# Performance work log

Measured on AMD Instinct MI355X. Metric: run time of the kernel, lower is better.

The kernel has to match this reference:

```python
import jax, jax.numpy as jnp
import numpy as np

N_NODES = 50000
N_EDGES = 1_600_000
DIMS = [3, 4096, 1024, 256, 64, 16]  # conv1..conv5 in/out widths


def setup_inputs() -> dict:
    key = jax.random.key(0)
    ks = jax.random.split(key, 2 + 2 * 6)
    x = jax.random.normal(ks[0], (N_NODES, DIMS[0]), jnp.float32)
    edge_index = jax.random.randint(ks[1], (2, N_EDGES), 0, N_NODES, jnp.int64)
    inp = {"x": x, "edge_index": edge_index}
    # GCNConv weights (lin has no bias fused; bias added after aggregation)
    for i in range(5):
        fi, fo = DIMS[i], DIMS[i + 1]
        inp[f"W{i+1}"] = jax.random.normal(ks[2 + 2 * i], (fi, fo), jnp.float32) / np.float32(np.sqrt(fi))
        inp[f"b{i+1}"] = jnp.zeros((fo,), jnp.float32)
    # final Linear(num_classes, 3)
    inp["Wl"] = jax.random.normal(ks[12], (DIMS[5], 3), jnp.float32) / np.float32(np.sqrt(DIMS[5]))
    inp["bl"] = jnp.zeros((3,), jnp.float32)
    return inp


def _gcn_layer(x, W, b, src, dst, dinv):
    """GCNConv: h = XW; out = D^-1/2 (A+I) D^-1/2 h + b (self-loops included)."""
    h = x @ W  # [N, out]
    norm = dinv[src] * dinv[dst]  # [E]
    agg = jax.ops.segment_sum(h[src] * norm[:, None], dst, num_segments=N_NODES)
    # self-loop term: norm_ii = dinv[i]^2
    return agg + h * (dinv * dinv)[:, None] + b


def reference(x, edge_index, W1, b1, W2, b2, W3, b3, W4, b4, W5, b5, Wl, bl):
    src, dst = edge_index[0], edge_index[1]
    # degree with self-loops (edge weights = 1), computed on target nodes
    deg = jax.ops.segment_sum(jnp.ones((N_EDGES,), x.dtype), dst, num_segments=N_NODES) + 1.0
    dinv = jax.lax.rsqrt(deg)
    h = _gcn_layer(x, W1, b1, src, dst, dinv)
    h = jax.nn.relu(h)  # dropout = identity in eval
    h = _gcn_layer(h, W2, b2, src, dst, dinv)
    h = jax.nn.relu(h)
    h = _gcn_layer(h, W3, b3, src, dst, dinv)
    h = jax.nn.relu(h)
    h = _gcn_layer(h, W4, b4, src, dst, dinv)
    h = jax.nn.relu(h)
    h = _gcn_layer(h, W5, b5, src, dst, dinv)
    # scatter_mean with broadcast index [0] -> global mean pool to [1, C]
    pooled = jnp.mean(h, axis=0, keepdims=True)
    return pooled @ Wl + bl  # [1, 3]
```

## Files before the change

### kernel.cpp

```cpp
#include <hip/hip_runtime.h>
#include <stdint.h>

#define NN 50000
#define NE 1600000

typedef _Float16 f16;
typedef __attribute__((ext_vector_type(8))) _Float16 h8;
typedef __attribute__((ext_vector_type(4))) _Float16 h4v;
typedef __attribute__((ext_vector_type(4))) float f32x4;
typedef __attribute__((ext_vector_type(2))) float f32x2;

union PackU { unsigned int u; f16 h[2]; };
union Pack4 { uint2 v; f16 h[4]; };
union Pack8 { uint4 v; f16 h[8]; };

__device__ __forceinline__ void storev(float* p, float v) { *p = v; }
__device__ __forceinline__ void storev(f16* p, float v) { *p = (f16)v; }

__device__ __forceinline__ unsigned char f2fp8(float v) {
    int pk = __builtin_amdgcn_cvt_pk_fp8_f32(v, v, 0, false);
    return (unsigned char)(pk & 0xff);
}

__global__ __launch_bounds__(256) void zero_int_kernel(int* __restrict__ p, int n) {
    int i = blockIdx.x * 256 + threadIdx.x;
    if (i < n) p[i] = 0;
}

__global__ __launch_bounds__(256) void count_kernel(const int* __restrict__ dst,
                                                    int* __restrict__ deg, int nE) {
    int e = blockIdx.x * 256 + threadIdx.x;
    if (e < nE) atomicAdd(&deg[dst[e]], 1);
}

__global__ __launch_bounds__(256) void dinv_kernel(const int* __restrict__ deg,
                                                   float* __restrict__ dinv, int n) {
    int i = blockIdx.x * 256 + threadIdx.x;
    if (i < n) dinv[i] = rsqrtf((float)deg[i] + 1.0f);
}

__global__ __launch_bounds__(256) void scan1_kernel(const int* __restrict__ cnt,
                                                    int* __restrict__ rs,
                                                    int* __restrict__ bsum, int n) {
    __shared__ int sm[256];
    int b = blockIdx.x, t = threadIdx.x, i = b * 256 + t;
    int v = (i < n) ? cnt[i] : 0;
    sm[t] = v;
    __syncthreads();
    for (int off = 1; off < 256; off <<= 1) {
        int x = 0;
        if (t >= off) x = sm[t - off];
        __syncthreads();
        if (t >= off) sm[t] += x;
        __syncthreads();
    }
    if (i < n) rs[i] = sm[t] - v;
    if (t == 255) bsum[b] = sm[255];
}

__global__ __launch_bounds__(256) void scan2_kernel(int* __restrict__ bsum,
                                                    int* __restrict__ rs, int nb, int n) {
    __shared__ int sm[256];
    int t = threadIdx.x;
    int v = (t < nb) ? bsum[t] : 0;
    sm[t] = v;
    __syncthreads();
    for (int off = 1; off < 256; off <<= 1) {
        int x = 0;
        if (t >= off) x = sm[t - off];
        __syncthreads();
        if (t >= off) sm[t] += x;
        __syncthreads();
    }
    if (t < nb) bsum[t] = sm[t] - v;
    if (t == 255) rs[n] = sm[255];
}

__global__ __launch_bounds__(256) void scan3_kernel(int* __restrict__ rs,
                                                    const int* __restrict__ bsum, int n) {
    int i = blockIdx.x * 256 + threadIdx.x;
    if (i < n) rs[i] += bsum[blockIdx.x];
}

__global__ __launch_bounds__(256) void fill_kernel(const int* __restrict__ src,
                                                   const int* __restrict__ dst,
                                                   const int* __restrict__ rs,
                                                   int* __restrict__ cur,
                                                   int* __restrict__ csr, int nE) {
    int e = blockIdx.x * 256 + threadIdx.x;
    if (e < nE) {
        int d = dst[e];
        int p = rs[d] + atomicAdd(&cur[d], 1);
        csr[p] = src[e];
    }
}

__global__ __launch_bounds__(256) void pack_w1_kernel(const float* __restrict__ W1,
                                                      const float* __restrict__ b1,
                                                      float* __restrict__ w1p) {
    int k = blockIdx.x * 256 + threadIdx.x;
    if (k < 4096) {
        w1p[k * 4 + 0] = W1[k];
        w1p[k * 4 + 1] = W1[4096 + k];
        w1p[k * 4 + 2] = W1[8192 + k];
        w1p[k * 4 + 3] = b1[k];
    }
}

__global__ __launch_bounds__(256) void tconv_kernel(const float* __restrict__ W,
                                                    f16* __restrict__ Wt,
                                                    int K, int N) {
    __shared__ float tile[32][33];
    int kb = blockIdx.y * 32, nb = blockIdx.x * 32;
    int tx = threadIdx.x & 31, ty = threadIdx.x >> 5;
    for (int r = ty; r < 32; r += 8)
        tile[r][tx] = W[(size_t)(kb + r) * N + nb + tx];
    __syncthreads();
    for (int r = ty; r < 32; r += 8)
        Wt[(size_t)(nb + r) * K + kb + tx] = (f16)tile[tx][r];
}

template <int F, int TPN, bool RELU, bool BIAS, typename InT, typename OutT>
__global__ __launch_bounds__(256) void agg_kernel(const InT* __restrict__ t,
                                                  const float* __restrict__ dinv,
                                                  const int* __restrict__ rs,
                                                  const int* __restrict__ csr,
                                                  const float* __restrict__ bias,
                                                  OutT* __restrict__ out, int out_ld,
                                                  int nNodes) {
    constexpr int NPB = 256 / TPN;
    constexpr int C   = F / TPN;
    static_assert(TPN * C == F, "F must be TPN*C");
    int node = blockIdx.x * NPB + (int)threadIdx.x / TPN;
    if (node >= nNodes) return;
    int lane = (int)threadIdx.x % TPN;

    float acc[C];
#pragma unroll
    for (int c = 0; c < C; ++c) acc[c] = 0.f;

    int e0 = rs[node], e1 = rs[node + 1];
    for (int e = e0; e < e1; ++e) {
        int s = csr[e];
        float w = dinv[s];
        const InT* tr = t + (size_t)s * F;
#pragma unroll
        for (int c = 0; c < C; ++c) acc[c] += w * (float)tr[lane + c * TPN];
    }
    float di = dinv[node];
    const InT* ti = t + (size_t)node * F;
    OutT* oi = out + (size_t)node * out_ld;
#pragma unroll
    for (int c = 0; c < C; ++c) {
        int col = lane + c * TPN;
        float v = di * acc[c] + di * di * (float)ti[col];
        if (BIAS) v += bias[col];
        if (RELU) v = fmaxf(v, 0.f);
        storev(oi + col, v);
    }
}

template <bool RELU>
__global__ __launch_bounds__(256) void agg_fp8_1024(const unsigned char* __restrict__ t,
                                                    const float* __restrict__ dinv,
                                                    const int* __restrict__ rs,
                                                    const int* __restrict__ csr,
                                                    const float* __restrict__ bias,
                                                    f16* __restrict__ out, int nNodes) {
    int node = blockIdx.x * 4 + ((int)threadIdx.x >> 6);
    if (node >= nNodes) return;
    int lane = (int)threadIdx.x & 63;

    float acc[16];
#pragma unroll
    for (int j = 0; j < 16; ++j) acc[j] = 0.f;

    int e0 = rs[node], e1 = rs[node + 1];
    int e = e0;
    for (; e + 1 < e1; e += 2) {
        int s0 = csr[e], s1 = csr[e + 1];
        float w0 = dinv[s0], w1 = dinv[s1];
        uint4 u0 = ((const uint4*)(t + (size_t)s0 * 1024))[lane];
        uint4 u1 = ((const uint4*)(t + (size_t)s1 * 1024))[lane];
        const unsigned int uw0[4] = {u0.x, u0.y, u0.z, u0.w};
        const unsigned int uw1[4] = {u1.x, u1.y, u1.z, u1.w};
#pragma unroll
        for (int q = 0; q < 4; ++q) {
            f32x2 l0 = __builtin_amdgcn_cvt_pk_f32_fp8((int)uw0[q], false);
            f32x2 h0 = __builtin_amdgcn_cvt_pk_f32_fp8((int)uw0[q], true);
            f32x2 l1 = __builtin_amdgcn_cvt_pk_f32_fp8((int)uw1[q], false);
            f32x2 h1 = __builtin_amdgcn_cvt_pk_f32_fp8((int)uw1[q], true);
            acc[q * 4 + 0] += w0 * l0.x + w1 * l1.x;
            acc[q * 4 + 1] += w0 * l0.y + w1 * l1.y;
            acc[q * 4 + 2] += w0 * h0.x + w1 * h1.x;
            acc[q * 4 + 3] += w0 * h0.y + w1 * h1.y;
        }
    }
    if (e < e1) {
        int s0 = csr[e];
        float w0 = dinv[s0];
        uint4 u0 = ((const uint4*)(t + (size_t)s0 * 1024))[lane];
        const unsigned int uw0[4] = {u0.x, u0.y, u0.z, u0.w};
#pragma unroll
        for (int q = 0; q < 4; ++q) {
            f32x2 l0 = __builtin_amdgcn_cvt_pk_f32_fp8((int)uw0[q], false);
            f32x2 h0 = __builtin_amdgcn_cvt_pk_f32_fp8((int)uw0[q], true);
            acc[q * 4 + 0] += w0 * l0.x;
            acc[q * 4 + 1] += w0 * l0.y;
            acc[q * 4 + 2] += w0 * h0.x;
            acc[q * 4 + 3] += w0 * h0.y;
        }
    }
    float di = dinv[node], di2 = di * di;
    uint4 us = ((const uint4*)(t + (size_t)node * 1024))[lane];
    const unsigned int uws[4] = {us.x, us.y, us.z, us.w};
    Pack8 o0, o1;
#pragma unroll
    for (int q = 0; q < 4; ++q) {
        f32x2 sl = __builtin_amdgcn_cvt_pk_f32_fp8((int)uws[q], false);
        f32x2 sh = __builtin_amdgcn_cvt_pk_f32_fp8((int)uws[q], true);
        float4 b = *(const float4*)(bias + 16 * lane + q * 4);
        float v0 = di * acc[q * 4 + 0] + di2 * sl.x + b.x;
        float v1 = di * acc[q * 4 + 1] + di2 * sl.y + b.y;
        float v2 = di * acc[q * 4 + 2] + di2 * sh.x + b.z;
        float v3 = di * acc[q * 4 + 3] + di2 * sh.y + b.w;
        if (RELU) {
            v0 = fmaxf(v0, 0.f); v1 = fmaxf(v1, 0.f);
            v2 = fmaxf(v2, 0.f); v3 = fmaxf(v3, 0.f);
        }
        Pack8& dst8 = (q < 2) ? o0 : o1;
        int base = (q & 1) * 4;
        dst8.h[base + 0] = (f16)v0;
        dst8.h[base + 1] = (f16)v1;
        dst8.h[base + 2] = (f16)v2;
        dst8.h[base + 3] = (f16)v3;
    }
    uint4* orow = (uint4*)(out + (size_t)node * 1024 + 16 * lane);
    orow[0] = o0.v;
    orow[1] = o1.v;
}

template <bool RELU>
__global__ __launch_bounds__(256) void agg_fp8_256(const unsigned char* __restrict__ t,
                                                   int in_ld,
                                                   const float* __restrict__ dinv,
                                                   const int* __restrict__ rs,
                                                   const int* __restrict__ csr,
                                                   const float* __restrict__ bias,
                                                   f16* __restrict__ out,
                                                   int out_ld, int nNodes) {
    int node = blockIdx.x * 4 + ((int)threadIdx.x >> 6);
    if (node >= nNodes) return;
    int lane = (int)threadIdx.x & 63;

    float acc0 = 0.f, acc1 = 0.f, acc2 = 0.f, acc3 = 0.f;
    int e0 = rs[node], e1 = rs[node + 1];
    int e = e0;
    for (; e + 1 < e1; e += 2) {
        int s0 = csr[e], s1 = csr[e + 1];
        float w0 = dinv[s0], w1 = dinv[s1];
        unsigned int u0 = ((const unsigned int*)(t + (size_t)s0 * in_ld))[lane];
        unsigned int u1 = ((const unsigned int*)(t + (size_t)s1 * in_ld))[lane];
        f32x2 l0 = __builtin_amdgcn_cvt_pk_f32_fp8((int)u0, false);
        f32x2 h0 = __builtin_amdgcn_cvt_pk_f32_fp8((int)u0, true);
        f32x2 l1 = __builtin_amdgcn_cvt_pk_f32_fp8((int)u1, false);
        f32x2 h1 = __builtin_amdgcn_cvt_pk_f32_fp8((int)u1, true);
        acc0 += w0 * l0.x + w1 * l1.x;
        acc1 += w0 * l0.y + w1 * l1.y;
        acc2 += w0 * h0.x + w1 * h1.x;
        acc3 += w0 * h0.y + w1 * h1.y;
    }
    if (e < e1) {
        int s0 = csr[e];
        float w0 = dinv[s0];
        unsigned int u0 = ((const unsigned int*)(t + (size_t)s0 * in_ld))[lane];
        f32x2 l0 = __builtin_amdgcn_cvt_pk_f32_fp8((int)u0, false);
        f32x2 h0 = __builtin_amdgcn_cvt_pk_f32_fp8((int)u0, true);
        acc0 += w0 * l0.x;
        acc1 += w0 * l0.y;
        acc2 += w0 * h0.x;
        acc3 += w0 * h0.y;
    }
    float di = dinv[node], di2 = di * di;
    unsigned int us = ((const unsigned int*)(t + (size_t)node * in_ld))[lane];
    f32x2 sl = __builtin_amdgcn_cvt_pk_f32_fp8((int)us, false);
    f32x2 sh = __builtin_amdgcn_cvt_pk_f32_fp8((int)us, true);
    float4 b = *(const float4*)(bias + 4 * lane);
    float v0 = di * acc0 + di2 * sl.x + b.x;
    float v1 = di * acc1 + di2 * sl.y + b.y;
    float v2 = di * acc2 + di2 * sh.x + b.z;
    float v3 = di * acc3 + di2 * sh.y + b.w;
    if (RELU) {
        v0 = fmaxf(v0, 0.f); v1 = fmaxf(v1, 0.f);
        v2 = fmaxf(v2, 0.f); v3 = fmaxf(v3, 0.f);
    }
    Pack4 pk;
    pk.h[0] = (f16)v0; pk.h[1] = (f16)v1; pk.h[2] = (f16)v2; pk.h[3] = (f16)v3;
    *(uint2*)(out + (size_t)node * out_ld + 4 * lane) = pk.v;
}

#define LDSTR 40

__global__ __launch_bounds__(512, 4) void gemm12_mfma10(const float* __restrict__ aggx,
                                                        const float* __restrict__ w1p,
                                                        const f16* __restrict__ Bt,
                                                        unsigned char* __restrict__ t2) {
    __shared__ f16 As[2 * 128 * LDSTR] __attribute__((aligned(16)));
    __shared__ f16 Bs[2 * 256 * LDSTR] __attribute__((aligned(16)));
    int tid = threadIdx.x;
    int m0  = blockIdx.x * 128;
    int n0c = blockIdx.y * 256;

    int mg = tid >> 3;
    int kg = tid & 7;
    float a0[2], a1[2], a2[2];
#pragma unroll
    for (int j = 0; j < 2; ++j) {
        int gm = m0 + mg * 2 + j;
        if (gm < NN) {
            a0[j] = aggx[gm * 3 + 0];
            a1[j] = aggx[gm * 3 + 1];
            a2[j] = aggx[gm * 3 + 2];
        } else {
            a0[j] = a1[j] = a2[j] = 0.f;
        }
    }

    int brow = tid >> 1;
    int bkof = (tid & 1) * 16;
    const f16* bbase = Bt + (size_t)(n0c + brow) * 4096 + bkof;

    int lane   = tid & 63;
    int wv     = tid >> 6;
    int wm     = (wv >> 2) * 64;
    int wn     = (wv & 3) * 64;
    int fr_m   = lane & 15;
    int khalf8 = (lane >> 4) * 8;

    auto stageA = [&](f16* dstAs, int kk) {
        int kb = kk + kg * 4;
        float4 wk0 = *(const float4*)(w1p + (size_t)(kb + 0) * 4);
        float4 wk1 = *(const float4*)(w1p + (size_t)(kb + 1) * 4);
        float4 wk2 = *(const float4*)(w1p + (size_t)(kb + 2) * 4);
        float4 wk3 = *(const float4*)(w1p + (size_t)(kb + 3) * 4);
#pragma unroll
        for (int j = 0; j < 2; ++j) {
            float h0 = fmaxf(a0[j] * wk0.x + a1[j] * wk0.y + a2[j] * wk0.z + wk0.w, 0.f);
            float h1 = fmaxf(a0[j] * wk1.x + a1[j] * wk1.y + a2[j] * wk1.z + wk1.w, 0.f);
            float h2 = fmaxf(a0[j] * wk2.x + a1[j] * wk2.y + a2[j] * wk2.z + wk2.w, 0.f);
            float h3 = fmaxf(a0[j] * wk3.x + a1[j] * wk3.y + a2[j] * wk3.z + wk3.w, 0.f);
            Pack4 pk;
            pk.h[0] = (f16)h0; pk.h[1] = (f16)h1; pk.h[2] = (f16)h2; pk.h[3] = (f16)h3;
            *(uint2*)(&dstAs[(mg * 2 + j) * LDSTR + kg * 4]) = pk.v;
        }
    };

    h8 pb0 = *(const h8*)(bbase);
    h8 pb1 = *(const h8*)(bbase + 8);
    stageA(As, 0);
    *(h8*)(&Bs[brow * LDSTR + bkof]) = pb0;
    *(h8*)(&Bs[brow * LDSTR + bkof + 8]) = pb1;
    pb0 = *(const h8*)(bbase + 32);
    pb1 = *(const h8*)(bbase + 32 + 8);

    f32x4 acc[4][4];
#pragma unroll
    for (int i = 0; i < 4; ++i)
#pragma unroll
        for (int j = 0; j < 4; ++j) acc[i][j] = (f32x4){0.f, 0.f, 0.f, 0.f};

    int p = 0;
    for (int k0 = 0; k0 < 4096; k0 += 32) {
        __syncthreads();
        const f16* Asc = As + p * (128 * LDSTR);
        const f16* Bsc = Bs + p * (256 * LDSTR);
        f16* Asn = As + (p ^ 1) * (128 * LDSTR);
        f16* Bsn = Bs + (p ^ 1) * (256 * LDSTR);

        int k1 = k0 + 32;
        if (k1 < 4096) {
            *(h8*)(&Bsn[brow * LDSTR + bkof]) = pb0;
            *(h8*)(&Bsn[brow * LDSTR + bkof + 8]) = pb1;
            stageA(Asn, k1);
        }

        h8 af[4];
#pragma unroll
        for (int mt = 0; mt < 4; ++mt)
            af[mt] = *(const h8*)(&Asc[(wm + mt * 16 + fr_m) * LDSTR + khalf8]);

        int k2 = k0 + 64;
        if (k2 < 4096) {
            pb0 = *(const h8*)(bbase + k2);
            pb1 = *(const h8*)(bbase + k2 + 8);
        }

#pragma unroll
        for (int nt = 0; nt < 4; ++nt) {
            h8 bf = *(const h8*)(&Bsc[(wn + nt * 16 + fr_m) * LDSTR + khalf8]);
#pragma unroll
            for (int mt = 0; mt < 4; ++mt)
                acc[mt][nt] = __builtin_amdgcn_mfma_f32_16x16x32_f16(af[mt], bf, acc[mt][nt], 0, 0, 0);
        }
        p ^= 1;
    }

#pragma unroll
    for (int mt = 0; mt < 4; ++mt) {
#pragma unroll
        for (int reg = 0; reg < 4; ++reg) {
            int gm = m0 + wm + mt * 16 + (lane >> 4) * 4 + reg;
            if (gm < NN) {
                unsigned char* orow = t2 + (size_t)gm * 1024 + n0c + wn + fr_m;
#pragma unroll
                for (int nt = 0; nt < 4; ++nt)
                    orow[nt * 16] = f2fp8(acc[mt][nt][reg]);
            }
        }
    }
}

__global__ __launch_bounds__(256) void gemm_mfma(const f16* __restrict__ A, int lda,
                                                 const f16* __restrict__ Bt, int K,
                                                 unsigned char* __restrict__ C, int ldc,
                                                 int M) {
    __shared__ f16 As[128 * LDSTR] __attribute__((aligned(16)));
    __shared__ f16 Bs[128 * LDSTR] __attribute__((aligned(16)));
    int tid = threadIdx.x;
    int m0 = blockIdx.y * 128;
    int n0 = blockIdx.x * 128;

    int row = tid >> 1;
    int kof = (tid & 1) * 16;
    int am  = m0 + row;
    if (am > M - 1) am = M - 1;

    int lane   = tid & 63;
    int wv     = tid >> 6;
    int fr_m   = lane & 15;
    int khalf8 = (lane >> 4) * 8;

    const f16* abase = A + (size_t)am * lda + kof;
    const f16* bbase = Bt + (size_t)(n0 + row) * K + kof;

    h8 pa0 = *(const h8*)(abase);
    h8 pa1 = *(const h8*)(abase + 8);
    h8 pb0 = *(const h8*)(bbase);
    h8 pb1 = *(const h8*)(bbase + 8);

    f32x4 acc[2][8];
#pragma unroll
    for (int i = 0; i < 2; ++i)
#pragma unroll
        for (int j = 0; j < 8; ++j) acc[i][j] = (f32x4){0.f, 0.f, 0.f, 0.f};

    for (int k0 = 0; k0 < K; k0 += 32) {
        *(h8*)(&As[row * LDSTR + kof]) = pa0;
        *(h8*)(&As[row * LDSTR + kof + 8]) = pa1;
        *(h8*)(&Bs[row * LDSTR + kof]) = pb0;
        *(h8*)(&Bs[row * LDSTR + kof + 8]) = pb1;
        __syncthreads();

        int kn = k0 + 32;
        if (kn < K) {
            pa0 = *(const h8*)(abase + kn);
            pa1 = *(const h8*)(abase + kn + 8);
            pb0 = *(const h8*)(bbase + kn);
            pb1 = *(const h8*)(bbase + kn + 8);
        }

        h8 af0 = *(const h8*)(&As[(wv * 32 + fr_m) * LDSTR + khalf8]);
        h8 af1 = *(const h8*)(&As[(wv * 32 + 16 + fr_m) * LDSTR + khalf8]);
#pragma unroll
        for (int nt = 0; nt < 8; ++nt) {
            h8 bf = *(const h8*)(&Bs[(nt * 16 + fr_m) * LDSTR + khalf8]);
            acc[0][nt] = __builtin_amdgcn_mfma_f32_16x16x32_f16(af0, bf, acc[0][nt], 0, 0, 0);
            acc[1][nt] = __builtin_amdgcn_mfma_f32_16x16x32_f16(af1, bf, acc[1][nt], 0, 0, 0);
        }
        __syncthreads();
    }

#pragma unroll
    for (int mt = 0; mt < 2; ++mt) {
#pragma unroll
        for (int reg = 0; reg < 4; ++reg) {
            int gm = m0 + wv * 32 + mt * 16 + (lane >> 4) * 4 + reg;
            if (gm < M) {
                unsigned char* orow = C + (size_t)gm * ldc + n0 + fr_m;
#pragma unroll
                for (int nt = 0; nt < 8; ++nt)
                    orow[nt * 16] = f2fp8(acc[mt][nt][reg]);
            }
        }
    }
}

#define BM 64
#define BN 64
#define BKS 16
__global__ __launch_bounds__(256) void gemm_f16A_kernel(const f16* __restrict__ A,
                                                        const float* __restrict__ B,
                                                        f16* __restrict__ C,
                                                        int M, int K, int N) {
    __shared__ float As[BKS][BM + 4];
    __shared__ float Bs[BKS][BN + 4];
    int tid = threadIdx.x;
    int tx = tid & 15;
    int ty = tid >> 4;
    int m0 = blockIdx.y * BM;
    int n0 = blockIdx.x * BN;

    float acc[4][4];
#pragma unroll
    for (int i = 0; i < 4; ++i)
#pragma unroll
        for (int j = 0; j < 4; ++j) acc[i][j] = 0.f;

    int lmA = tid >> 2;
    int lkA = (tid & 3) * 4;
    int lkB = tid >> 4;
    int lnB = (tid & 15) * 4;

    for (int k0 = 0; k0 < K; k0 += BKS) {
        int gm = m0 + lmA;
        if (gm > M - 1) gm = M - 1;
        h4v av = *(const h4v*)(A + (size_t)gm * K + k0 + lkA);
        As[lkA + 0][lmA] = (float)av.x;
        As[lkA + 1][lmA] = (float)av.y;
        As[lkA + 2][lmA] = (float)av.z;
        As[lkA + 3][lmA] = (float)av.w;
        float4 bv = *reinterpret_cast<const float4*>(B + (size_t)(k0 + lkB) * N + n0 + lnB);
        *reinterpret_cast<float4*>(&Bs[lkB][lnB]) = bv;
        __syncthreads();

#pragma unroll
        for (int k = 0; k < BKS; ++k) {
            float4 a4 = *reinterpret_cast<const float4*>(&As[k][ty * 4]);
            float4 b4 = *reinterpret_cast<const float4*>(&Bs[k][tx * 4]);
            float a[4] = {a4.x, a4.y, a4.z, a4.w};
            float b[4] = {b4.x, b4.y, b4.z, b4.w};
#pragma unroll
            for (int i = 0; i < 4; ++i)
#pragma unroll
                for (int j = 0; j < 4; ++j) acc[i][j] += a[i] * b[j];
        }
        __syncthreads();
    }

#pragma unroll
    for (int i = 0; i < 4; ++i) {
        int m = m0 + ty * 4 + i;
        if (m < M) {
            Pack4 pk;
            pk.h[0] = (f16)acc[i][0]; pk.h[1] = (f16)acc[i][1];
            pk.h[2] = (f16)acc[i][2]; pk.h[3] = (f16)acc[i][3];
            *reinterpret_cast<uint2*>(C + (size_t)m * N + n0 + tx * 4) = pk.v;
        }
    }
}

__global__ __launch_bounds__(256) void gemm5_kernel(const f16* __restrict__ h4,
                                                    const float* __restrict__ W5,
                                                    f16* __restrict__ t5, int nNodes) {
    int idx = blockIdx.x * 256 + threadIdx.x;
    int i = idx >> 4, j = idx & 15;
    if (i >= nNodes) return;
    const f16* a = h4 + (size_t)i * 64;
    float s = 0.f;
#pragma unroll
    for (int k = 0; k < 64; ++k) s += (float)a[k] * W5[k * 16 + j];
    t5[idx] = (f16)s;
}

__global__ __launch_bounds__(256) void pool_kernel(const float* __restrict__ h5,
                                                   float* __restrict__ pool) {
    __shared__ float red[256];
    int c = blockIdx.x;
    float s = 0.f;
    for (int i = threadIdx.x; i < NN; i += 256) s += h5[(size_t)i * 16 + c];
    red[threadIdx.x] = s;
    __syncthreads();
    for (int off = 128; off > 0; off >>= 1) {
        if ((int)threadIdx.x < off) red[threadIdx.x] += red[threadIdx.x + off];
        __syncthreads();
    }
    if (threadIdx.x == 0) pool[c] = red[0];
}

__global__ void final_kernel(const float* __restrict__ pool, const float* __restrict__ Wl,
                             const float* __restrict__ bl, float* __restrict__ out) {
    int j = threadIdx.x;
    if (j < 3) {
        float s = 0.f;
#pragma unroll
        for (int c = 0; c < 16; ++c) s += pool[c] * Wl[c * 3 + j];
        out[j] = s * (1.0f / (float)NN) + bl[j];
    }
}

extern "C" void kernel_launch(void* const* d_in, const int* in_sizes, int n_in,
                              void* d_out, int out_size, void* d_ws, size_t ws_size,
                              hipStream_t stream) {
    (void)in_sizes; (void)n_in; (void)out_size; (void)ws_size;

    const float* x  = (const float*)d_in[0];
    const int*   ei = (const int*)d_in[1];
    const float* W1 = (const float*)d_in[2];
    const float* b1 = (const float*)d_in[3];
    const float* W2 = (const float*)d_in[4];
    const float* b2 = (const float*)d_in[5];
    const float* W3 = (const float*)d_in[6];
    const float* b3 = (const float*)d_in[7];
    const float* W4 = (const float*)d_in[8];
    const float* b4 = (const float*)d_in[9];
    const float* W5 = (const float*)d_in[10];
    const float* b5 = (const float*)d_in[11];
    const float* Wl = (const float*)d_in[12];
    const float* bl = (const float*)d_in[13];
    float* out = (float*)d_out;

    const int* srcp = ei;
    const int* dstp = ei + NE;

    char* p = (char*)d_ws;
    auto carve = [&](size_t bytes) {
        char* r = p;
        p += (bytes + 255) & ~(size_t)255;
        return r;
    };
    int*   deg  = (int*)carve(NN * 4);
    int*   cur  = (int*)carve(NN * 4);
    int*   rs   = (int*)carve((NN + 1) * 4);
    int*   bsum = (int*)carve(256 * 4);
    int*   csr  = (int*)carve((size_t)NE * 4);
    float* dinv = (float*)carve(NN * 4);
    float* aggx = (float*)carve((size_t)NN * 3 * 4);
    float* pool = (float*)carve(16 * 4);
    float* w1p  = (float*)carve((size_t)4096 * 4 * 4);
    f16*   w2t  = (f16*)carve((size_t)1024 * 4096 * 2);
    f16*   w3t  = (f16*)carve((size_t)256 * 1024 * 2);
    unsigned char* tbuf = (unsigned char*)carve((size_t)NN * 1024);
    f16*   h2   = (f16*)carve((size_t)NN * 1024 * 2);
    f16*   h3   = (f16*)carve((size_t)NN * 256 * 2);
    f16*   h4   = (f16*)carve((size_t)NN * 64 * 2);
    float* h5   = (float*)carve((size_t)NN * 16 * 4);
    f16*   tf16 = (f16*)tbuf;

    const int NB = (NN + 255) / 256;

    zero_int_kernel<<<NB, 256, 0, stream>>>(deg, NN);
    zero_int_kernel<<<NB, 256, 0, stream>>>(cur, NN);
    count_kernel<<<(NE + 255) / 256, 256, 0, stream>>>(dstp, deg, NE);
    dinv_kernel<<<NB, 256, 0, stream>>>(deg, dinv, NN);
    scan1_kernel<<<NB, 256, 0, stream>>>(deg, rs, bsum, NN);
    scan2_kernel<<<1, 256, 0, stream>>>(bsum, rs, NB, NN);
    scan3_kernel<<<NB, 256, 0, stream>>>(rs, bsum, NN);
    fill_kernel<<<(NE + 255) / 256, 256, 0, stream>>>(srcp, dstp, rs, cur, csr, NE);

    pack_w1_kernel<<<16, 256, 0, stream>>>(W1, b1, w1p);
    tconv_kernel<<<dim3(1024 / 32, 4096 / 32), 256, 0, stream>>>(W2, w2t, 4096, 1024);
    tconv_kernel<<<dim3(256 / 32, 1024 / 32), 256, 0, stream>>>(W3, w3t, 1024, 256);

    agg_kernel<3, 1, false, false, float, float><<<NB, 256, 0, stream>>>(
        x, dinv, rs, csr, nullptr, aggx, 3, NN);

    const int MB2 = (NN + 127) / 128;

    gemm12_mfma10<<<dim3(MB2, 4), 512, 0, stream>>>(aggx, w1p, w2t, tbuf);
    agg_fp8_1024<true><<<(NN + 3) / 4, 256, 0, stream>>>(
        tbuf, dinv, rs, csr, b2, h2, NN);

    gemm_mfma<<<dim3(2, MB2), 256, 0, stream>>>(
        h2, 1024, w3t, 1024, tbuf, 256, NN);
    agg_fp8_256<true><<<(NN + 3) / 4, 256, 0, stream>>>(
        tbuf, 256, dinv, rs, csr, b3, h3, 256, NN);

    gemm_f16A_kernel<<<dim3(1, (NN + BM - 1) / BM), 256, 0, stream>>>(
        h3, W4, tf16, NN, 256, 64);
    agg_kernel<64, 64, true, true, f16, f16><<<(NN + 3) / 4, 256, 0, stream>>>(
        tf16, dinv, rs, csr, b4, h4, 64, NN);

    gemm5_kernel<<<(NN * 16 + 255) / 256, 256, 0, stream>>>(h4, W5, tf16, NN);
    agg_kernel<16, 16, false, true, f16, float><<<(NN + 15) / 16, 256, 0, stream>>>(
        tf16, dinv, rs, csr, b5, h5, 16, NN);

    pool_kernel<<<16, 256, 0, stream>>>(h5, pool);
    final_kernel<<<1, 64, 0, stream>>>(pool, Wl, bl, out);
}
```

Baseline: 1.570 ms.

## Use MFMA for layer-4 GEMM, vectorize layer-5 GEMM, parallelize layer-1 aggregation

Replaces the scalar-FP32 tiled GEMM for layer 4 (256->64) with an MFMA f16 kernel that uses a pre-transposed f16 copy of W4 and register-prefetched LDS tiles. Layer-5's GEMM now computes all 16 outputs per thread with vector loads and stores instead of one output per thread. The layer-1 aggregation uses 3 threads per node instead of 1. These target small kernels on the tail of the pipeline, so the overall effect is limited, and casting W4 to f16 slightly changes precision.

Result: no change. 1.561 ms (-0.6%).

```diff
diff --git a/kernel.cpp b/kernel.cpp
--- a/kernel.cpp
+++ b/kernel.cpp
@@ -131,6 +131,7 @@
     constexpr int NPB = 256 / TPN;
     constexpr int C   = F / TPN;
     static_assert(TPN * C == F, "F must be TPN*C");
+    if ((int)threadIdx.x >= NPB * TPN) return;
     int node = blockIdx.x * NPB + (int)threadIdx.x / TPN;
     if (node >= nNodes) return;
     int lane = (int)threadIdx.x % TPN;
@@ -495,66 +496,84 @@
     }
 }
 
-#define BM 64
-#define BN 64
-#define BKS 16
-__global__ __launch_bounds__(256) void gemm_f16A_kernel(const f16* __restrict__ A,
-                                                        const float* __restrict__ B,
-                                                        f16* __restrict__ C,
-                                                        int M, int K, int N) {
-    __shared__ float As[BKS][BM + 4];
-    __shared__ float Bs[BKS][BN + 4];
+__global__ __launch_bounds__(256) void gemm_mfma_n64(const f16* __restrict__ A,
+                                                     const f16* __restrict__ Bt,
+                                                     f16* __restrict__ C, int M) {
+    __shared__ f16 As[128 * LDSTR] __attribute__((aligned(16)));
+    __shared__ f16 Bs[64 * LDSTR] __attribute__((aligned(16)));
     int tid = threadIdx.x;
-    int tx = tid & 15;
-    int ty = tid >> 4;
-    int m0 = blockIdx.y * BM;
-    int n0 = blockIdx.x * BN;
-
-    float acc[4][4];
-#pragma unroll
-    for (int i = 0; i < 4; ++i)
-#pragma unroll
-        for (int j = 0; j < 4; ++j) acc[i][j] = 0.f;
-
-    int lmA = tid >> 2;
-    int lkA = (tid & 3) * 4;
-    int lkB = tid >> 4;
-    int lnB = (tid & 15) * 4;
-
-    for (int k0 = 0; k0 < K; k0 += BKS) {
-        int gm = m0 + lmA;
-        if (gm > M - 1) gm = M - 1;
-        h4v av = *(const h4v*)(A + (size_t)gm * K + k0 + lkA);
-        As[lkA + 0][lmA] = (float)av.x;
-        As[lkA + 1][lmA] = (float)av.y;
-        As[lkA + 2][lmA] = (float)av.z;
-        As[lkA + 3][lmA] = (float)av.w;
-        float4 bv = *reinterpret_cast<const float4*>(B + (size_t)(k0 + lkB) * N + n0 + lnB);
-        *reinterpret_cast<float4*>(&Bs[lkB][lnB]) = bv;
-        __syncthreads();
-
-#pragma unroll
-        for (int k = 0; k < BKS; ++k) {
-            float4 a4 = *reinterpret_cast<const float4*>(&As[k][ty * 4]);
-            float4 b4 = *reinterpret_cast<const float4*>(&Bs[k][tx * 4]);
-            float a[4] = {a4.x, a4.y, a4.z, a4.w};
-            float b[4] = {b4.x, b4.y, b4.z, b4.w};
-#pragma unroll
-            for (int i = 0; i < 4; ++i)
-#pragma unroll
-                for (int j = 0; j < 4; ++j) acc[i][j] += a[i] * b[j];
-        }
-        __syncthreads();
-    }
-
-#pragma unroll
-    for (int i = 0; i < 4; ++i) {
-        int m = m0 + ty * 4 + i;
-        if (m < M) {
-            Pack4 pk;
-            pk.h[0] = (f16)acc[i][0]; pk.h[1] = (f16)acc[i][1];
-            pk.h[2] = (f16)acc[i][2]; pk.h[3] = (f16)acc[i][3];
-            *reinterpret_cast<uint2*>(C + (size_t)m * N + n0 + tx * 4) = pk.v;
+    int m0 = blockIdx.x * 128;
+
+    int row = tid >> 1;
+    int kof = (tid & 1) * 16;
+    int am  = m0 + row;
+    if (am > M - 1) am = M - 1;
+
+    int lane   = tid & 63;
+    int wv     = tid >> 6;
+    int fr_m   = lane & 15;
+    int khalf8 = (lane >> 4) * 8;
+
+    const f16* abase = A + (size_t)am * 256 + kof;
+    int brow = (tid & 127) >> 1;
+    const f16* bbase = Bt + (size_t)brow * 256 + kof;
+    bool doB = tid < 128;
+
+    h8 pa0 = *(const h8*)(abase);
+    h8 pa1 = *(const h8*)(abase + 8);
+    h8 pb0, pb1;
+    if (doB) {
+        pb0 = *(const h8*)(bbase);
+        pb1 = *(const h8*)(bbase + 8);
+    }
+
+    f32x4 acc[2][4];
+#pragma unroll
+    for (int i = 0; i < 2; ++i)
+#pragma unroll
+        for (int j = 0; j < 4; ++j) acc[i][j] = (f32x4){0.f, 0.f, 0.f, 0.f};
+
+    for (int k0 = 0; k0 < 256; k0 += 32) {
+        *(h8*)(&As[row * LDSTR + kof]) = pa0;
+        *(h8*)(&As[row * LDSTR + kof + 8]) = pa1;
+        if (doB) {
+            *(h8*)(&Bs[brow * LDSTR + kof]) = pb0;
+            *(h8*)(&Bs[brow * LDSTR + kof + 8]) = pb1;
+        }
+        __syncthreads();
+
+        int kn = k0 + 32;
+        if (kn < 256) {
+            pa0 = *(const h8*)(abase + kn);
+            pa1 = *(const h8*)(abase + kn + 8);
+            if (doB) {
+                pb0 = *(const h8*)(bbase + kn);
+                pb1 = *(const h8*)(bbase + kn + 8);
+            }
+        }
+
+        h8 af0 = *(const h8*)(&As[(wv * 32 + fr_m) * LDSTR + khalf8]);
+        h8 af1 = *(const h8*)(&As[(wv * 32 + 16 + fr_m) * LDSTR + khalf8]);
+#pragma unroll
+        for (int nt = 0; nt < 4; ++nt) {
+            h8 bf = *(const h8*)(&Bs[(nt * 16 + fr_m) * LDSTR + khalf8]);
+            acc[0][nt] = __builtin_amdgcn_mfma_f32_16x16x32_f16(af0, bf, acc[0][nt], 0, 0, 0);
+            acc[1][nt] = __builtin_amdgcn_mfma_f32_16x16x32_f16(af1, bf, acc[1][nt], 0, 0, 0);
+        }
+        __syncthreads();
+    }
+
+#pragma unroll
+    for (int mt = 0; mt < 2; ++mt) {
+#pragma unroll
+        for (int reg = 0; reg < 4; ++reg) {
+            int gm = m0 + wv * 32 + mt * 16 + (lane >> 4) * 4 + reg;
+            if (gm < M) {
+                f16* orow = C + (size_t)gm * 64 + fr_m;
+#pragma unroll
+                for (int nt = 0; nt < 4; ++nt)
+                    orow[nt * 16] = (f16)acc[mt][nt][reg];
+            }
         }
     }
 }
@@ -562,14 +581,29 @@
 __global__ __launch_bounds__(256) void gemm5_kernel(const f16* __restrict__ h4,
                                                     const float* __restrict__ W5,
                                                     f16* __restrict__ t5, int nNodes) {
-    int idx = blockIdx.x * 256 + threadIdx.x;
-    int i = idx >> 4, j = idx & 15;
+    int i = blockIdx.x * 256 + threadIdx.x;
     if (i >= nNodes) return;
-    const f16* a = h4 + (size_t)i * 64;
-    float s = 0.f;
-#pragma unroll
-    for (int k = 0; k < 64; ++k) s += (float)a[k] * W5[k * 16 + j];
-    t5[idx] = (f16)s;
+    const h8* a = (const h8*)(h4 + (size_t)i * 64);
+    float s[16];
+#pragma unroll
+    for (int j = 0; j < 16; ++j) s[j] = 0.f;
+#pragma unroll
+    for (int kb = 0; kb < 8; ++kb) {
+        h8 av = a[kb];
+#pragma unroll
+        for (int t = 0; t < 8; ++t) {
+            float aval = (float)av[t];
+            const float* wrow = W5 + (kb * 8 + t) * 16;
+#pragma unroll
+            for (int j = 0; j < 16; ++j) s[j] += aval * wrow[j];
+        }
+    }
+    Pack8 o0, o1;
+#pragma unroll
+    for (int j = 0; j < 8; ++j) { o0.h[j] = (f16)s[j]; o1.h[j] = (f16)s[j + 8]; }
+    uint4* op = (uint4*)(t5 + (size_t)i * 16);
+    op[0] = o0.v;
+    op[1] = o1.v;
 }
 
 __global__ __launch_bounds__(256) void pool_kernel(const float* __restrict__ h5,
@@ -639,6 +673,7 @@
     float* w1p  = (float*)carve((size_t)4096 * 4 * 4);
     f16*   w2t  = (f16*)carve((size_t)1024 * 4096 * 2);
     f16*   w3t  = (f16*)carve((size_t)256 * 1024 * 2);
+    f16*   w4t  = (f16*)carve((size_t)64 * 256 * 2);
     unsigned char* tbuf = (unsigned char*)carve((size_t)NN * 1024);
     f16*   h2   = (f16*)carve((size_t)NN * 1024 * 2);
     f16*   h3   = (f16*)carve((size_t)NN * 256 * 2);
@@ -660,8 +695,9 @@
     pack_w1_kernel<<<16, 256, 0, stream>>>(W1, b1, w1p);
     tconv_kernel<<<dim3(1024 / 32, 4096 / 32), 256, 0, stream>>>(W2, w2t, 4096, 1024);
     tconv_kernel<<<dim3(256 / 32, 1024 / 32), 256, 0, stream>>>(W3, w3t, 1024, 256);
-
-    agg_kernel<3, 1, false, false, float, float><<<NB, 256, 0, stream>>>(
+    tconv_kernel<<<dim3(64 / 32, 256 / 32), 256, 0, stream>>>(W4, w4t, 256, 64);
+
+    agg_kernel<3, 3, false, false, float, float><<<(NN + 84) / 85, 256, 0, stream>>>(
         x, dinv, rs, csr, nullptr, aggx, 3, NN);
 
     const int MB2 = (NN + 127) / 128;
@@ -675,12 +711,11 @@
     agg_fp8_256<true><<<(NN + 3) / 4, 256, 0, stream>>>(
         tbuf, 256, dinv, rs, csr, b3, h3, 256, NN);
 
-    gemm_f16A_kernel<<<dim3(1, (NN + BM - 1) / BM), 256, 0, stream>>>(
-        h3, W4, tf16, NN, 256, 64);
+    gemm_mfma_n64<<<MB2, 256, 0, stream>>>(h3, w4t, tf16, NN);
     agg_kernel<64, 64, true, true, f16, f16><<<(NN + 3) / 4, 256, 0, stream>>>(
         tf16, dinv, rs, csr, b4, h4, 64, NN);
 
-    gemm5_kernel<<<(NN * 16 + 255) / 256, 256, 0, stream>>>(h4, W5, tf16, NN);
+    gemm5_kernel<<<(NN + 255) / 256, 256, 0, stream>>>(h4, W5, tf16, NN);
     agg_kernel<16, 16, false, true, f16, float><<<(NN + 15) / 16, 256, 0, stream>>>(
         tf16, dinv, rs, csr, b5, h5, 16, NN);
 
```
